# Optimization experiments

Hardware: AMD Instinct MI355X
Metric: run time of the kernel (lower is better)

Reference implementation:

```python
import jax, jax.numpy as jnp
import numpy as np

NEG_INF = -1000000000.0
INPUT_SIZE = 1024
HIDDEN_SIZE = 64
B, S = 8, 2048


def setup_inputs() -> dict:
    key = jax.random.key(0)
    ks = jax.random.split(key, 8)
    scale = 1.0 / np.sqrt(INPUT_SIZE)
    inp = {
        "input": jax.random.normal(ks[0], (B, S, INPUT_SIZE), dtype=jnp.float32),
        "mask": jax.random.randint(ks[1], (B, S, S), 0, 2, dtype=jnp.int32),
        "W_q": jax.random.uniform(ks[2], (HIDDEN_SIZE, INPUT_SIZE), jnp.float32, -scale, scale),
        "b_q": jax.random.uniform(ks[3], (HIDDEN_SIZE,), jnp.float32, -scale, scale),
        "W_k": jax.random.uniform(ks[4], (HIDDEN_SIZE, INPUT_SIZE), jnp.float32, -scale, scale),
        "b_k": jax.random.uniform(ks[5], (HIDDEN_SIZE,), jnp.float32, -scale, scale),
        "W_v": jax.random.uniform(ks[6], (HIDDEN_SIZE, INPUT_SIZE), jnp.float32, -scale, scale),
        "b_v": jax.random.uniform(ks[7], (HIDDEN_SIZE,), jnp.float32, -scale, scale),
    }
    return inp


def reference(input, mask, W_q, b_q, W_k, b_k, W_v, b_v):
    inv_sqrt_d = 1.0 / np.sqrt(HIDDEN_SIZE)
    # Q/K/V projections: torch Linear is x @ W.T + b
    q = jnp.einsum('bsi,hi->bsh', input, W_q) + b_q  # (B,S,H)
    k = jnp.einsum('bsi,hi->bsh', input, W_k) + b_k
    v = jnp.einsum('bsi,hi->bsh', input, W_v) + b_v
    scores = jnp.einsum('bqh,bkh->bqk', q, k) * inv_sqrt_d  # (B,S,S)
    scores = jnp.where(mask == 0, NEG_INF, scores)
    probs = jax.nn.softmax(scores, axis=-1)
    return jnp.einsum('bqk,bkh->bqh', probs, v)  # (B,S,H)
```

## Files before the change

### kernel.cpp

```cpp
#include <hip/hip_runtime.h>

typedef __bf16 bf16;
typedef bf16 bf16x4 __attribute__((ext_vector_type(4)));
typedef bf16 bf16x8 __attribute__((ext_vector_type(8)));
typedef float floatx4 __attribute__((ext_vector_type(4)));
typedef unsigned int u32;

#define B_ 8
#define S_ 2048
#define I_ 1024
#define H_ 64
#define NEG_INF_ -1000000000.0f

__device__ __forceinline__ void async_cp16(bf16* lds_base, const bf16* g_base, int lane) {
    __builtin_amdgcn_global_load_lds(
        (const __attribute__((address_space(1))) u32*)(g_base + lane * 8),
        (__attribute__((address_space(3))) u32*)lds_base, 16, 0, 0);
}

__global__ void conv_w(const float* __restrict__ Wq, const float* __restrict__ bq,
                       const float* __restrict__ Wk, const float* __restrict__ bk,
                       const float* __restrict__ Wv, const float* __restrict__ bv,
                       bf16* __restrict__ Wc, float* __restrict__ bc) {
    int idx = blockIdx.x * 256 + threadIdx.x;
    int n = idx >> 10, i = idx & 1023;
    float v;
    if (n < 64)       v = Wq[n * I_ + i] * 0.125f;
    else if (n < 128) v = Wk[(n - 64) * I_ + i];
    else              v = Wv[(n - 128) * I_ + i];
    Wc[idx] = (bf16)v;
    if (idx < 192) {
        float bb = (idx < 64) ? bq[idx] * 0.125f
                 : (idx < 128) ? bk[idx - 64] : bv[idx - 128];
        bc[idx] = bb;
    }
}

__global__ __launch_bounds__(256, 4) void qkv_gemm(const float* __restrict__ X,
                                                   const bf16* __restrict__ Wc,
                                                   const float* __restrict__ bc,
                                                   bf16* __restrict__ Qd,
                                                   bf16* __restrict__ Kd2,
                                                   bf16* __restrict__ Vt2) {
    __shared__ __align__(16) bf16 Xs[16 * 72];
    __shared__ __align__(16) bf16 Ws[192 * 72];

    int tid = threadIdx.x;
    int w = tid >> 6, lane = tid & 63;
    int n = lane & 15, g = lane >> 4;
    int m0 = blockIdx.x * 16;

    floatx4 zero4 = {0.0f, 0.0f, 0.0f, 0.0f};
    floatx4 acc[3];
#pragma unroll
    for (int t = 0; t < 3; ++t) acc[t] = zero4;

    int xrow = tid >> 4, xq = tid & 15;
    const float* xsrc = X + (size_t)(m0 + xrow) * I_ + xq * 4;
    bf16* xdst = Xs + xrow * 72 + xq * 4;

    for (int kk0 = 0; kk0 < I_; kk0 += 64) {
        float4 xv = *(const float4*)(xsrc + kk0);
        bf16x4 xb;
        xb[0] = (bf16)xv.x; xb[1] = (bf16)xv.y; xb[2] = (bf16)xv.z; xb[3] = (bf16)xv.w;
        *(bf16x4*)xdst = xb;
#pragma unroll
        for (int i = 0; i < 6; ++i) {
            int cid = i * 256 + tid;
            int wrow = cid >> 3, wc = cid & 7;
            *(bf16x8*)(Ws + wrow * 72 + wc * 8) =
                *(const bf16x8*)(Wc + (size_t)wrow * I_ + kk0 + wc * 8);
        }
        __syncthreads();
#pragma unroll
        for (int ks = 0; ks < 2; ++ks) {
            bf16x8 xa = *(bf16x8*)(Xs + n * 72 + ks * 32 + g * 8);
#pragma unroll
            for (int nt = 0; nt < 3; ++nt) {
                bf16x8 wb = *(bf16x8*)(Ws + (w * 48 + nt * 16 + n) * 72 + ks * 32 + g * 8);
                acc[nt] = __builtin_amdgcn_mfma_f32_16x16x32_bf16(xa, wb, acc[nt], 0, 0, 0);
            }
        }
        __syncthreads();
    }

    int b = m0 >> 11;
    int sb = (m0 & 2047) + g * 4;
#pragma unroll
    for (int nt = 0; nt < 3; ++nt) {
        int ng = w * 48 + nt * 16 + n;
        float bias = bc[ng];
        if (ng < 64) {
#pragma unroll
            for (int r = 0; r < 4; ++r)
                Qd[(size_t)(b * S_ + sb + r) * H_ + ng] = (bf16)(acc[nt][r] + bias);
        } else if (ng < 128) {
            int hc = (ng - 64) >> 3, j = (ng - 64) & 7;
#pragma unroll
            for (int r = 0; r < 4; ++r)
                Kd2[((size_t)(b * 8 + hc) * S_ + sb + r) * 8 + j] = (bf16)(acc[nt][r] + bias);
        } else {
            int hh = ng - 128, kc = sb >> 3, jj = sb & 7;
            bf16x4 pk;
#pragma unroll
            for (int r = 0; r < 4; ++r) pk[r] = (bf16)(acc[nt][r] + bias);
            *(bf16x4*)(Vt2 + ((size_t)(b * 256 + kc) * 64 + hh) * 8 + jj) = pk;
        }
    }
}

__global__ __launch_bounds__(256, 4) void attn(const bf16* __restrict__ Qd,
                                               const bf16* __restrict__ Kd2,
                                               const bf16* __restrict__ Vt2,
                                               const int* __restrict__ mask,
                                               float* __restrict__ po,
                                               float* __restrict__ pml) {
    __shared__ __align__(16) bf16 regA[8704];
    __shared__ __align__(16) bf16 Vs[16 * 528];

    int tid = threadIdx.x;
    int w = tid >> 6, lane = tid & 63;
    int n = lane & 15, g = lane >> 4;
    int bid = blockIdx.x;
    int ksp = bid & 3;
    int qt = (bid >> 2) & 31;
    int b = bid >> 7;
    int q0 = qt * 64;

    const bf16* qptr = Qd + (size_t)(b * S_ + q0 + w * 16 + n) * H_ + g * 8;
    bf16x8 qa0 = *(const bf16x8*)qptr;
    bf16x8 qa1 = *(const bf16x8*)(qptr + 32);

    floatx4 zero4 = {0.0f, 0.0f, 0.0f, 0.0f};
    floatx4 o[4];
#pragma unroll
    for (int t = 0; t < 4; ++t) o[t] = zero4;
    float m_i[4], l_i[4];
#pragma unroll
    for (int r = 0; r < 4; ++r) { m_i[r] = -INFINITY; l_i[r] = 0.0f; }

    for (int kt = ksp * 4; kt < ksp * 4 + 4; ++kt) {
#pragma unroll
        for (int j = 0; j < 4; ++j) {
            int hc = w * 2 + (j >> 1), p = j & 1;
            async_cp16(regA + hc * 1040 + p * 512,
                       Kd2 + ((size_t)(b * 8 + hc) * S_ + kt * 128 + p * 64) * 8, lane);
        }
#pragma unroll
        for (int j = 0; j < 4; ++j) {
            int kcl = w * 4 + j;
            async_cp16(Vs + kcl * 528,
                       Vt2 + ((size_t)(b * 256 + kt * 16 + kcl) * 64) * 8, lane);
        }
        const int* mb = mask + (size_t)(b * S_ + q0 + w * 16 + g * 4) * S_ + kt * 128 + n;
        int mreg[4][8];
#pragma unroll
        for (int r = 0; r < 4; ++r)
#pragma unroll
            for (int nt = 0; nt < 8; ++nt)
                mreg[r][nt] = mb[(size_t)r * S_ + nt * 16];
        __syncthreads();

        floatx4 s[8];
#pragma unroll
        for (int nt = 0; nt < 8; ++nt) {
            floatx4 a = zero4;
            a = __builtin_amdgcn_mfma_f32_16x16x32_bf16(
                    qa0, *(const bf16x8*)(regA + g * 1040 + (nt * 16 + n) * 8), a, 0, 0, 0);
            a = __builtin_amdgcn_mfma_f32_16x16x32_bf16(
                    qa1, *(const bf16x8*)(regA + (4 + g) * 1040 + (nt * 16 + n) * 8), a, 0, 0, 0);
            s[nt] = a;
        }

#pragma unroll
        for (int r = 0; r < 4; ++r)
#pragma unroll
            for (int nt = 0; nt < 8; ++nt)
                if (mreg[r][nt] == 0) s[nt][r] = NEG_INF_;
#pragma unroll
        for (int r = 0; r < 4; ++r) {
            float tm = s[0][r];
#pragma unroll
            for (int nt = 1; nt < 8; ++nt) tm = fmaxf(tm, s[nt][r]);
#pragma unroll
            for (int off = 1; off < 16; off <<= 1) tm = fmaxf(tm, __shfl_xor(tm, off, 64));
            float mn = fmaxf(m_i[r], tm);
            float alpha = __expf(m_i[r] - mn);
            m_i[r] = mn;
            float rs = 0.0f;
#pragma unroll
            for (int nt = 0; nt < 8; ++nt) {
                float p = __expf(s[nt][r] - mn);
                s[nt][r] = p;
                rs += p;
            }
#pragma unroll
            for (int off = 1; off < 16; off <<= 1) rs += __shfl_xor(rs, off, 64);
            l_i[r] = l_i[r] * alpha + rs;
#pragma unroll
            for (int ht = 0; ht < 4; ++ht) o[ht][r] *= alpha;
        }
        __syncthreads();

#pragma unroll
        for (int r = 0; r < 4; ++r)
#pragma unroll
            for (int nt = 0; nt < 8; ++nt)
                regA[(w * 16 + g * 4 + r) * 136 + nt * 16 + n] = (bf16)s[nt][r];
        __syncthreads();

#pragma unroll
        for (int k0 = 0; k0 < 4; ++k0) {
            bf16x8 pa = *(bf16x8*)(regA + (w * 16 + n) * 136 + k0 * 32 + g * 8);
#pragma unroll
            for (int ht = 0; ht < 4; ++ht) {
                bf16x8 vb = *(bf16x8*)(Vs + (k0 * 4 + g) * 528 + (ht * 16 + n) * 8);
                o[ht] = __builtin_amdgcn_mfma_f32_16x16x32_bf16(pa, vb, o[ht], 0, 0, 0);
            }
        }
        __syncthreads();
    }

    float* pb = po + (size_t)bid * 4096;
#pragma unroll
    for (int ht = 0; ht < 4; ++ht)
#pragma unroll
        for (int r = 0; r < 4; ++r)
            pb[(w * 16 + g * 4 + r) * 64 + ht * 16 + n] = o[ht][r];
    if (n == 0) {
#pragma unroll
        for (int r = 0; r < 4; ++r) {
            pml[(size_t)bid * 128 + w * 16 + g * 4 + r] = m_i[r];
            pml[(size_t)bid * 128 + 64 + w * 16 + g * 4 + r] = l_i[r];
        }
    }
}

__global__ __launch_bounds__(256) void reduce_o(const float* __restrict__ po,
                                                const float* __restrict__ pml,
                                                float* __restrict__ out) {
    int idx = blockIdx.x * 256 + threadIdx.x;
    int h = idx & 63, q = idx >> 6;
    int b = q >> 11, qq = q & 2047;
    int qt = qq >> 6, ql = qq & 63;
    int bid0 = (b * 32 + qt) * 4;
    float mj[4], lj[4], M = -INFINITY;
#pragma unroll
    for (int j = 0; j < 4; ++j) {
        mj[j] = pml[(size_t)(bid0 + j) * 128 + ql];
        lj[j] = pml[(size_t)(bid0 + j) * 128 + 64 + ql];
        M = fmaxf(M, mj[j]);
    }
    float num = 0.0f, den = 0.0f;
#pragma unroll
    for (int j = 0; j < 4; ++j) {
        float sc = __expf(mj[j] - M);
        den += lj[j] * sc;
        num += po[(size_t)(bid0 + j) * 4096 + ql * 64 + h] * sc;
    }
    out[(size_t)q * 64 + h] = num / den;
}

extern "C" void kernel_launch(void* const* d_in, const int* in_sizes, int n_in,
                              void* d_out, int out_size, void* d_ws, size_t ws_size,
                              hipStream_t stream) {
    const float* X    = (const float*)d_in[0];
    const int*   mask = (const int*)d_in[1];
    const float* Wq   = (const float*)d_in[2];
    const float* bq   = (const float*)d_in[3];
    const float* Wk   = (const float*)d_in[4];
    const float* bk   = (const float*)d_in[5];
    const float* Wv   = (const float*)d_in[6];
    const float* bv   = (const float*)d_in[7];
    float* out = (float*)d_out;

    char* p = (char*)d_ws;
    bf16* Qd   = (bf16*)p;  p += (size_t)B_ * S_ * H_ * 2;
    bf16* Kd2  = (bf16*)p;  p += (size_t)B_ * S_ * H_ * 2;
    bf16* Vt2  = (bf16*)p;  p += (size_t)B_ * S_ * H_ * 2;
    bf16* Wc   = (bf16*)p;  p += (size_t)192 * 1024 * 2;
    float* bc  = (float*)p; p += 1024;
    float* po  = (float*)p; p += (size_t)1024 * 4096 * 4;
    float* pml = (float*)p; p += (size_t)1024 * 128 * 4;

    conv_w<<<dim3(768), dim3(256), 0, stream>>>(Wq, bq, Wk, bk, Wv, bv, Wc, bc);
    qkv_gemm<<<dim3(1024), dim3(256), 0, stream>>>(X, Wc, bc, Qd, Kd2, Vt2);
    attn<<<dim3(1024), dim3(256), 0, stream>>>(Qd, Kd2, Vt2, mask, po, pml);
    reduce_o<<<dim3(4096), dim3(256), 0, stream>>>(po, pml, out);
}
```

Baseline: 277.3 us.

## Enlarge QKV GEMM tiles with pre-padded weight slabs loaded via async LDS copies

The QKV projection GEMM now processes 32 rows per block with 128-wide K steps, and each wave computes 6 output tiles instead of 3. The weights are pre-laid out by conv_w into padded per-K-slab chunks so they can be streamed directly into LDS with global_load_lds. This halves the number of blocks and cuts weight reloads per row, at the cost of a much larger LDS footprint, fewer resident blocks and more accumulator registers. In the attention kernel, the mask loads are also issued before the K/V async copies to start the global mask traffic earlier.

```diff
diff --git a/kernel.cpp b/kernel.cpp
--- a/kernel.cpp
+++ b/kernel.cpp
@@ -21,14 +21,15 @@
 __global__ void conv_w(const float* __restrict__ Wq, const float* __restrict__ bq,
                        const float* __restrict__ Wk, const float* __restrict__ bk,
                        const float* __restrict__ Wv, const float* __restrict__ bv,
-                       bf16* __restrict__ Wc, float* __restrict__ bc) {
+                       bf16* __restrict__ Wc2, float* __restrict__ bc) {
     int idx = blockIdx.x * 256 + threadIdx.x;
     int n = idx >> 10, i = idx & 1023;
     float v;
     if (n < 64)       v = Wq[n * I_ + i] * 0.125f;
     else if (n < 128) v = Wk[(n - 64) * I_ + i];
     else              v = Wv[(n - 128) * I_ + i];
-    Wc[idx] = (bf16)v;
+    int s = i >> 7, kl = i & 127;
+    Wc2[(size_t)s * 26112 + n * 136 + kl] = (bf16)v;
     if (idx < 192) {
         float bb = (idx < 64) ? bq[idx] * 0.125f
                  : (idx < 128) ? bk[idx - 64] : bv[idx - 128];
@@ -36,48 +37,57 @@
     }
 }
 
-__global__ __launch_bounds__(256, 4) void qkv_gemm(const float* __restrict__ X,
-                                                   const bf16* __restrict__ Wc,
+__global__ __launch_bounds__(256, 2) void qkv_gemm(const float* __restrict__ X,
+                                                   const bf16* __restrict__ Wc2,
                                                    const float* __restrict__ bc,
                                                    bf16* __restrict__ Qd,
                                                    bf16* __restrict__ Kd2,
                                                    bf16* __restrict__ Vt2) {
-    __shared__ __align__(16) bf16 Xs[16 * 72];
-    __shared__ __align__(16) bf16 Ws[192 * 72];
+    __shared__ __align__(16) bf16 Xs[32 * 136];
+    __shared__ __align__(16) bf16 Ws[26112];
 
     int tid = threadIdx.x;
     int w = tid >> 6, lane = tid & 63;
     int n = lane & 15, g = lane >> 4;
-    int m0 = blockIdx.x * 16;
+    int m0 = blockIdx.x * 32;
+    int mt = w & 1, nh = (w >> 1) * 96;
 
     floatx4 zero4 = {0.0f, 0.0f, 0.0f, 0.0f};
-    floatx4 acc[3];
-#pragma unroll
-    for (int t = 0; t < 3; ++t) acc[t] = zero4;
-
-    int xrow = tid >> 4, xq = tid & 15;
-    const float* xsrc = X + (size_t)(m0 + xrow) * I_ + xq * 4;
-    bf16* xdst = Xs + xrow * 72 + xq * 4;
-
-    for (int kk0 = 0; kk0 < I_; kk0 += 64) {
-        float4 xv = *(const float4*)(xsrc + kk0);
-        bf16x4 xb;
-        xb[0] = (bf16)xv.x; xb[1] = (bf16)xv.y; xb[2] = (bf16)xv.z; xb[3] = (bf16)xv.w;
-        *(bf16x4*)xdst = xb;
-#pragma unroll
-        for (int i = 0; i < 6; ++i) {
-            int cid = i * 256 + tid;
-            int wrow = cid >> 3, wc = cid & 7;
-            *(bf16x8*)(Ws + wrow * 72 + wc * 8) =
-                *(const bf16x8*)(Wc + (size_t)wrow * I_ + kk0 + wc * 8);
-        }
-        __syncthreads();
-#pragma unroll
-        for (int ks = 0; ks < 2; ++ks) {
-            bf16x8 xa = *(bf16x8*)(Xs + n * 72 + ks * 32 + g * 8);
-#pragma unroll
-            for (int nt = 0; nt < 3; ++nt) {
-                bf16x8 wb = *(bf16x8*)(Ws + (w * 48 + nt * 16 + n) * 72 + ks * 32 + g * 8);
+    floatx4 acc[6];
+#pragma unroll
+    for (int t = 0; t < 6; ++t) acc[t] = zero4;
+
+    int xrow = tid >> 3, xcb = (tid & 7) * 16;
+    const float* xsrc = X + (size_t)(m0 + xrow) * I_ + xcb;
+    bf16* xdst = Xs + xrow * 136 + xcb;
+
+    for (int s = 0; s < 8; ++s) {
+        const float* xp = xsrc + s * 128;
+        float4 x0 = *(const float4*)(xp);
+        float4 x1 = *(const float4*)(xp + 4);
+        float4 x2 = *(const float4*)(xp + 8);
+        float4 x3 = *(const float4*)(xp + 12);
+#pragma unroll
+        for (int i = 0; i < 13; ++i) {
+            int inst = i * 4 + w;
+            if (inst < 51)
+                async_cp16(Ws + inst * 512, Wc2 + (size_t)s * 26112 + inst * 512, lane);
+        }
+        bf16x8 b0, b1;
+        b0[0] = (bf16)x0.x; b0[1] = (bf16)x0.y; b0[2] = (bf16)x0.z; b0[3] = (bf16)x0.w;
+        b0[4] = (bf16)x1.x; b0[5] = (bf16)x1.y; b0[6] = (bf16)x1.z; b0[7] = (bf16)x1.w;
+        b1[0] = (bf16)x2.x; b1[1] = (bf16)x2.y; b1[2] = (bf16)x2.z; b1[3] = (bf16)x2.w;
+        b1[4] = (bf16)x3.x; b1[5] = (bf16)x3.y; b1[6] = (bf16)x3.z; b1[7] = (bf16)x3.w;
+        *(bf16x8*)xdst = b0;
+        *(bf16x8*)(xdst + 8) = b1;
+        __syncthreads();
+
+#pragma unroll
+        for (int ks = 0; ks < 4; ++ks) {
+            bf16x8 xa = *(bf16x8*)(Xs + (mt * 16 + n) * 136 + ks * 32 + g * 8);
+#pragma unroll
+            for (int nt = 0; nt < 6; ++nt) {
+                bf16x8 wb = *(bf16x8*)(Ws + (nh + nt * 16 + n) * 136 + ks * 32 + g * 8);
                 acc[nt] = __builtin_amdgcn_mfma_f32_16x16x32_bf16(xa, wb, acc[nt], 0, 0, 0);
             }
         }
@@ -85,10 +95,10 @@
     }
 
     int b = m0 >> 11;
-    int sb = (m0 & 2047) + g * 4;
-#pragma unroll
-    for (int nt = 0; nt < 3; ++nt) {
-        int ng = w * 48 + nt * 16 + n;
+    int sb = (m0 & 2047) + mt * 16 + g * 4;
+#pragma unroll
+    for (int nt = 0; nt < 6; ++nt) {
+        int ng = nh + nt * 16 + n;
         float bias = bc[ng];
         if (ng < 64) {
 #pragma unroll
@@ -140,6 +150,13 @@
     for (int r = 0; r < 4; ++r) { m_i[r] = -INFINITY; l_i[r] = 0.0f; }
 
     for (int kt = ksp * 4; kt < ksp * 4 + 4; ++kt) {
+        const int* mb = mask + (size_t)(b * S_ + q0 + w * 16 + g * 4) * S_ + kt * 128 + n;
+        int mreg[4][8];
+#pragma unroll
+        for (int r = 0; r < 4; ++r)
+#pragma unroll
+            for (int nt = 0; nt < 8; ++nt)
+                mreg[r][nt] = mb[(size_t)r * S_ + nt * 16];
 #pragma unroll
         for (int j = 0; j < 4; ++j) {
             int hc = w * 2 + (j >> 1), p = j & 1;
@@ -152,13 +169,6 @@
             async_cp16(Vs + kcl * 528,
                        Vt2 + ((size_t)(b * 256 + kt * 16 + kcl) * 64) * 8, lane);
         }
-        const int* mb = mask + (size_t)(b * S_ + q0 + w * 16 + g * 4) * S_ + kt * 128 + n;
-        int mreg[4][8];
-#pragma unroll
-        for (int r = 0; r < 4; ++r)
-#pragma unroll
-            for (int nt = 0; nt < 8; ++nt)
-                mreg[r][nt] = mb[(size_t)r * S_ + nt * 16];
         __syncthreads();
 
         floatx4 s[8];
@@ -278,13 +288,13 @@
     bf16* Qd   = (bf16*)p;  p += (size_t)B_ * S_ * H_ * 2;
     bf16* Kd2  = (bf16*)p;  p += (size_t)B_ * S_ * H_ * 2;
     bf16* Vt2  = (bf16*)p;  p += (size_t)B_ * S_ * H_ * 2;
-    bf16* Wc   = (bf16*)p;  p += (size_t)192 * 1024 * 2;
+    bf16* Wc2  = (bf16*)p;  p += (size_t)8 * 26112 * 2;
     float* bc  = (float*)p; p += 1024;
     float* po  = (float*)p; p += (size_t)1024 * 4096 * 4;
     float* pml = (float*)p; p += (size_t)1024 * 128 * 4;
 
-    conv_w<<<dim3(768), dim3(256), 0, stream>>>(Wq, bq, Wk, bk, Wv, bv, Wc, bc);
-    qkv_gemm<<<dim3(1024), dim3(256), 0, stream>>>(X, Wc, bc, Qd, Kd2, Vt2);
+    conv_w<<<dim3(768), dim3(256), 0, stream>>>(Wq, bq, Wk, bk, Wv, bv, Wc2, bc);
+    qkv_gemm<<<dim3(512), dim3(256), 0, stream>>>(X, Wc2, bc, Qd, Kd2, Vt2);
     attn<<<dim3(1024), dim3(256), 0, stream>>>(Qd, Kd2, Vt2, mask, po, pml);
     reduce_o<<<dim3(4096), dim3(256), 0, stream>>>(po, pml, out);
 }
```

Result: faster. 267.1 us (-3.7%).
